# Optimization experiments

Measured on AMD Instinct MI355X. Metric: run time of the kernel, lower is better.

## Reference

```python
import jax, jax.numpy as jnp
import numpy as np

N_LEVELS = 127.0  # 2^(8-1)-1, symmetric signed int8


def _ste_round_clip(x, scale, lo, hi):
    """Fake-quantize x to integers in [lo,hi] at given scale, straight-through estimator."""
    q = jnp.clip(jnp.round(x / scale), lo, hi) * scale
    return x + jax.lax.stop_gradient(q - x)


def quant_act(x):
    """Per-tensor symmetric int8 activation quantization (QuantAct)."""
    scale = jax.lax.stop_gradient(jnp.max(jnp.abs(x)) / N_LEVELS)
    xq = _ste_round_clip(x, scale, -N_LEVELS - 1.0, N_LEVELS)
    return xq, scale


def quant_linear(xq, act_scale, w, b):
    """Per-tensor symmetric int8 weight quantization + bias quantized at act*weight scale (QuantLinear)."""
    w_scale = jax.lax.stop_gradient(jnp.max(jnp.abs(w)) / N_LEVELS)
    wq = _ste_round_clip(w, w_scale, -N_LEVELS, N_LEVELS)
    bias_scale = act_scale * w_scale
    bq = b + jax.lax.stop_gradient(jnp.round(b / bias_scale) * bias_scale - b)
    out = xq @ wq.T + bq  # equivalent to int8 GEMM accumulated in int32, dequantized
    return out, w_scale


def setup_inputs() -> dict:
    key = jax.random.key(0)
    ks = jax.random.split(key, 7)
    B, D_IN, D_H, D_OUT = 512, 9216, 4096, 1000  # AlexNet head dims
    s1 = 1.0 / np.sqrt(D_IN)
    s2 = 1.0 / np.sqrt(D_H)
    return {
        "x": jax.random.normal(ks[0], (B, D_IN), jnp.float32),
        "w1": jax.random.normal(ks[1], (D_H, D_IN), jnp.float32) * s1,
        "b1": jax.random.normal(ks[2], (D_H,), jnp.float32) * 0.01,
        "w2": jax.random.normal(ks[3], (D_H, D_H), jnp.float32) * s2,
        "b2": jax.random.normal(ks[4], (D_H,), jnp.float32) * 0.01,
        "w3": jax.random.normal(ks[5], (D_OUT, D_H), jnp.float32) * s2,
        "b3": jax.random.normal(ks[6], (D_OUT,), jnp.float32) * 0.01,
    }


def reference(x, w1, b1, w2, b2, w3, b3):
    # quant_act -> quant_fc1 -> ReLU -> (Dropout: eval=identity) -> quant_act1 -> quant_fc2 -> ReLU -> quant_act2 -> quant_fc3
    xq, a_s = quant_act(x)
    h, _ = quant_linear(xq, a_s, w1, b1)
    h = jax.nn.relu(h)
    hq, a_s = quant_act(h)
    h, _ = quant_linear(hq, a_s, w2, b2)
    h = jax.nn.relu(h)
    hq, a_s = quant_act(h)
    out, _ = quant_linear(hq, a_s, w3, b3)
    return out
```

## Files before the change

kernel.cpp:

```cpp
#include <hip/hip_runtime.h>
#include <hip/hip_bf16.h>

typedef __attribute__((ext_vector_type(4))) int   int32x4;
typedef __attribute__((ext_vector_type(4))) float float4v;


__global__ void init_stats(float* stats) {
    if (threadIdx.x < 64) stats[threadIdx.x] = 0.0f;
}

__global__ void maxabs_kernel(const float* __restrict__ src, long nchunk, float* __restrict__ out) {
    const int tid  = threadIdx.x;
    const int lane = tid & 63;
    const int wid  = tid >> 6;
    __shared__ float red[4];
    float m0 = 0.0f, m1 = 0.0f, m2 = 0.0f, m3 = 0.0f;
    for (long c = blockIdx.x; c < nchunk; c += gridDim.x) {
        const float4v* p = (const float4v*)src + c * 1024 + tid;
        float4v v0 = p[0], v1 = p[256], v2 = p[512], v3 = p[768];
        m0 = fmaxf(m0, fmaxf(fmaxf(fabsf(v0.x), fabsf(v0.y)), fmaxf(fabsf(v0.z), fabsf(v0.w))));
        m1 = fmaxf(m1, fmaxf(fmaxf(fabsf(v1.x), fabsf(v1.y)), fmaxf(fabsf(v1.z), fabsf(v1.w))));
        m2 = fmaxf(m2, fmaxf(fmaxf(fabsf(v2.x), fabsf(v2.y)), fmaxf(fabsf(v2.z), fabsf(v2.w))));
        m3 = fmaxf(m3, fmaxf(fmaxf(fabsf(v3.x), fabsf(v3.y)), fmaxf(fabsf(v3.z), fabsf(v3.w))));
    }
    float m = fmaxf(fmaxf(m0, m1), fmaxf(m2, m3));
    #pragma unroll
    for (int off = 32; off; off >>= 1) m = fmaxf(m, __shfl_xor(m, off, 64));
    if (lane == 0) red[wid] = m;
    __syncthreads();
    if (tid == 0) {
        float r = fmaxf(fmaxf(red[0], red[1]), fmaxf(red[2], red[3]));
        atomicMax((unsigned int*)out, __float_as_uint(r));
    }
}

__global__ void quant_kernel(const float* __restrict__ src, signed char* __restrict__ dst,
                             const float* __restrict__ stats, int slot,
                             float lo, float hi, long nchunk) {
    const float scale = stats[slot] / 127.0f;
    const int tid = threadIdx.x;
    for (long c = blockIdx.x; c < nchunk; c += gridDim.x) {
        const float4v* p = (const float4v*)src + c * 1024 + tid;
        int* d = (int*)dst + c * 1024 + tid;
        float4v v0 = p[0], v1 = p[256], v2 = p[512], v3 = p[768];
        float4v vs[4] = {v0, v1, v2, v3};
        int packed[4];
        #pragma unroll
        for (int j = 0; j < 4; ++j) {
            float4v v = vs[j];
            int b0 = (int)fminf(fmaxf(rintf(v.x / scale), lo), hi);
            int b1 = (int)fminf(fmaxf(rintf(v.y / scale), lo), hi);
            int b2 = (int)fminf(fmaxf(rintf(v.z / scale), lo), hi);
            int b3 = (int)fminf(fmaxf(rintf(v.w / scale), lo), hi);
            packed[j] = (b0 & 0xff) | ((b1 & 0xff) << 8) | ((b2 & 0xff) << 16) | ((b3 & 0xff) << 24);
        }
        d[0]   = packed[0];
        d[256] = packed[1];
        d[512] = packed[2];
        d[768] = packed[3];
    }
}

template <int BM, int BN, int FR, int FC, bool RELUMAX>
__global__ __launch_bounds__(256, 2)
void gemm_q8(const signed char* __restrict__ A, const signed char* __restrict__ Bw,
             const float* __restrict__ bias, float* __restrict__ stats,
             int a_slot, int w_slot, int h_slot,
             float* __restrict__ C, int K, int Ncols) {
    constexpr int BK = 64;
    constexpr int NWC = BN / (FC * 16);
    constexpr int L = BM / 64 + BN / 64;
    static_assert((BM / (FR * 16)) * (BN / (FC * 16)) == 4, "4 waves");
    constexpr int LDS_A = BM * BK;
    constexpr int LDS_TILE = (BM + BN) * BK;
    __shared__ __align__(16) signed char lds[3][LDS_TILE];

    const int tid  = threadIdx.x;
    const int wid  = tid >> 6;
    const int lane = tid & 63;
    const int wr   = wid / NWC;
    const int wc   = wid % NWC;

    const long brow = (long)blockIdx.y * BM;
    const long bcol = (long)blockIdx.x * BN;

    const signed char* Ab = A  + brow * K;
    const signed char* Bb = Bw + bcol * K;

    const int srow = tid >> 2;
    const int scb  = (tid & 3) * 16;
    const int scsrc = scb ^ (((srow >> 1) & 3) << 4);

    int32x4 zero = {0, 0, 0, 0};
    int32x4 acc[FR][FC];
    #pragma unroll
    for (int r = 0; r < FR; ++r)
        #pragma unroll
        for (int c = 0; c < FC; ++c) acc[r][c] = zero;

    auto stage = [&](int buf, int kt) {
        #pragma unroll
        for (int i = 0; i < BM / 64; ++i) {
            __builtin_amdgcn_global_load_lds(
                (const __attribute__((address_space(1))) void*)(Ab + (long)(srow + i * 64) * K + kt + scsrc),
                (__attribute__((address_space(3))) void*)(&lds[buf][(srow + i * 64) * BK + scb]),
                16, 0, 0);
        }
        #pragma unroll
        for (int i = 0; i < BN / 64; ++i) {
            __builtin_amdgcn_global_load_lds(
                (const __attribute__((address_space(1))) void*)(Bb + (long)(srow + i * 64) * K + kt + scsrc),
                (__attribute__((address_space(3))) void*)(&lds[buf][LDS_A + (srow + i * 64) * BK + scb]),
                16, 0, 0);
        }
    };

    const int nt = K / BK;
    stage(0, 0);
    if (nt > 1) stage(1, BK);

    for (int t = 0; t < nt; ++t) {
        if (t + 1 < nt) {
            asm volatile("s_waitcnt vmcnt(%0)\n\ts_barrier" :: "n"(L) : "memory");
        } else {
            asm volatile("s_waitcnt vmcnt(0)\n\ts_barrier" ::: "memory");
        }
        if (t + 2 < nt) stage((t + 2) % 3, (t + 2) * BK);

        const signed char* la = &lds[t % 3][0];
        const signed char* lb = &lds[t % 3][LDS_A];
        int32x4 af[FR], bf[FC];
        #pragma unroll
        for (int r = 0; r < FR; ++r) {
            const int row = wr * (FR * 16) + r * 16 + (lane & 15);
            const int col = ((lane >> 4) * 16) ^ (((row >> 1) & 3) << 4);
            af[r] = *(const int32x4*)(la + row * BK + col);
        }
        #pragma unroll
        for (int c = 0; c < FC; ++c) {
            const int row = wc * (FC * 16) + c * 16 + (lane & 15);
            const int col = ((lane >> 4) * 16) ^ (((row >> 1) & 3) << 4);
            bf[c] = *(const int32x4*)(lb + row * BK + col);
        }

        #pragma unroll
        for (int r = 0; r < FR; ++r)
            #pragma unroll
            for (int c = 0; c < FC; ++c)
                acc[r][c] = __builtin_amdgcn_mfma_i32_16x16x64_i8(af[r], bf[c], acc[r][c], 0, 0, 0);
    }

    const float sa = stats[a_slot] / 127.0f;
    const float sw = stats[w_slot] / 127.0f;
    const float s  = sa * sw;
    float lmax = 0.0f;
    #pragma unroll
    for (int c = 0; c < FC; ++c) {
        const long col = bcol + wc * (FC * 16) + c * 16 + (lane & 15);
        const bool colok = (col < Ncols);
        float bint = 0.0f;
        if (colok) bint = rintf(bias[col] / s);
        #pragma unroll
        for (int r = 0; r < FR; ++r) {
            #pragma unroll
            for (int j = 0; j < 4; ++j) {
                const long row = brow + wr * (FR * 16) + r * 16 + (lane >> 4) * 4 + j;
                float v = ((float)acc[r][c][j] + bint) * s;
                if (RELUMAX) v = fmaxf(v, 0.0f);
                if (colok) C[row * Ncols + col] = v;
                if (RELUMAX) lmax = fmaxf(lmax, v);
            }
        }
    }
    if (RELUMAX) {
        __shared__ float red[4];
        #pragma unroll
        for (int off = 32; off; off >>= 1) lmax = fmaxf(lmax, __shfl_xor(lmax, off, 64));
        if (lane == 0) red[wid] = lmax;
        __syncthreads();
        if (tid == 0) {
            float r = fmaxf(fmaxf(red[0], red[1]), fmaxf(red[2], red[3]));
            atomicMax((unsigned int*)&stats[h_slot], __float_as_uint(r));
        }
    }
}

static inline long lminl(long a, long b) { return a < b ? a : b; }

extern "C" void kernel_launch(void* const* d_in, const int* in_sizes, int n_in,
                              void* d_out, int out_size, void* d_ws, size_t ws_size,
                              hipStream_t stream) {
    const float* x  = (const float*)d_in[0];
    const float* w1 = (const float*)d_in[1];
    const float* b1 = (const float*)d_in[2];
    const float* w2 = (const float*)d_in[3];
    const float* b2 = (const float*)d_in[4];
    const float* w3 = (const float*)d_in[5];
    const float* b3 = (const float*)d_in[6];
    float* out = (float*)d_out;

    constexpr int B = 512, DIN = 9216, DH = 4096, DOUT = 1000;

    char* ws = (char*)d_ws;
    float*       stats = (float*)ws;
    signed char* xq    = (signed char*)(ws + 256);
    signed char* w1q   = xq  + (size_t)B * DIN;
    signed char* w2q   = w1q + (size_t)DH * DIN;
    signed char* w3q   = w2q + (size_t)DH * DH;
    signed char* h1q   = w3q + (size_t)1024 * DH;
    signed char* h2q   = h1q + (size_t)B * DH;
    float*       hbuf  = (float*)(h2q + (size_t)B * DH);
    const size_t need  = 256 + (size_t)B*DIN + (size_t)DH*DIN + (size_t)DH*DH + (size_t)1024*DH
                       + 2*(size_t)B*DH + (size_t)B*DH*4;
    if (ws_size < need) return;

    init_stats<<<1, 64, 0, stream>>>(stats);

    auto launch_maxabs = [&](const float* p, long n, int slot) {
        long nchunk = n / 4096;
        int blocks = (int)lminl(nchunk, 2048);
        maxabs_kernel<<<blocks, 256, 0, stream>>>(p, nchunk, stats + slot);
    };
    auto launch_quant = [&](const float* p, signed char* q, long n, int slot, float lo) {
        long nchunk = n / 4096;
        int blocks = (int)lminl(nchunk, 2048);
        quant_kernel<<<blocks, 256, 0, stream>>>(p, q, stats, slot, lo, 127.0f, nchunk);
    };

    launch_maxabs(x, (long)B * DIN, 0);
    launch_quant(x, xq, (long)B * DIN, 0, -128.0f);
    launch_maxabs(w1, (long)DH * DIN, 1);
    launch_quant(w1, w1q, (long)DH * DIN, 1, -127.0f);
    launch_maxabs(w2, (long)DH * DH, 2);
    launch_quant(w2, w2q, (long)DH * DH, 2, -127.0f);
    launch_maxabs(w3, (long)DOUT * DH, 3);
    launch_quant(w3, w3q, (long)DOUT * DH, 3, -127.0f);

    gemm_q8<64, 128, 2, 4, true><<<dim3(DH / 128, B / 64), 256, 0, stream>>>(
        xq, w1q, b1, stats, 0, 1, 4, hbuf, DIN, DH);
    launch_quant(hbuf, h1q, (long)B * DH, 4, -128.0f);

    gemm_q8<64, 128, 2, 4, true><<<dim3(DH / 128, B / 64), 256, 0, stream>>>(
        h1q, w2q, b2, stats, 4, 2, 5, hbuf, DH, DH);
    launch_quant(hbuf, h2q, (long)B * DH, 5, -128.0f);

    gemm_q8<64, 64, 2, 2, false><<<dim3(16, B / 64), 256, 0, stream>>>(
        h2q, w3q, b3, stats, 5, 3, 0, out, DH, DOUT);
}
```

Baseline: 545.0 us.

## Split-K int8 GEMMs with atomic int32 accumulation and separate epilogue kernels

Each GEMM now splits K four ways across gridDim.z and accumulates int32 partials into a zeroed workspace with atomicAdd. Separate finish kernels then apply the bias, dequantize, run ReLU and compute the max-abs statistic. The goal is more blocks to fill the GPU, since the grids were only 256 and 128 blocks before, and launch_bounds are raised for occupancy. The cost is extra zeroing and finish passes, heavy atomic traffic on the output, and more launches.

```diff
diff --git a/kernel.cpp b/kernel.cpp
--- a/kernel.cpp
+++ b/kernel.cpp
@@ -7,6 +7,13 @@
 
 __global__ void init_stats(float* stats) {
     if (threadIdx.x < 64) stats[threadIdx.x] = 0.0f;
+}
+
+__global__ void zero_kernel(int32x4* __restrict__ p, long n4) {
+    long i = (long)blockIdx.x * blockDim.x + threadIdx.x;
+    long stride = (long)gridDim.x * blockDim.x;
+    int32x4 z = {0, 0, 0, 0};
+    for (; i < n4; i += stride) p[i] = z;
 }
 
 __global__ void maxabs_kernel(const float* __restrict__ src, long nchunk, float* __restrict__ out) {
@@ -61,12 +68,10 @@
     }
 }
 
-template <int BM, int BN, int FR, int FC, bool RELUMAX>
-__global__ __launch_bounds__(256, 2)
+template <int BM, int BN, int FR, int FC>
+__global__ __launch_bounds__(256, 4)
 void gemm_q8(const signed char* __restrict__ A, const signed char* __restrict__ Bw,
-             const float* __restrict__ bias, float* __restrict__ stats,
-             int a_slot, int w_slot, int h_slot,
-             float* __restrict__ C, int K, int Ncols) {
+             int* __restrict__ Acc, int K, int kslice, int ldacc) {
     constexpr int BK = 64;
     constexpr int NWC = BN / (FC * 16);
     constexpr int L = BM / 64 + BN / 64;
@@ -81,11 +86,12 @@
     const int wr   = wid / NWC;
     const int wc   = wid % NWC;
 
-    const long brow = (long)blockIdx.y * BM;
-    const long bcol = (long)blockIdx.x * BN;
-
-    const signed char* Ab = A  + brow * K;
-    const signed char* Bb = Bw + bcol * K;
+    const int brow  = blockIdx.y * BM;
+    const int bcol  = blockIdx.x * BN;
+    const int kbase = blockIdx.z * kslice;
+
+    const signed char* Ab = A  + (long)brow * K + kbase;
+    const signed char* Bb = Bw + (long)bcol * K + kbase;
 
     const int srow = tid >> 2;
     const int scb  = (tid & 3) * 16;
@@ -115,7 +121,7 @@
         }
     };
 
-    const int nt = K / BK;
+    const int nt = kslice / BK;
     stage(0, 0);
     if (nt > 1) stage(1, BK);
 
@@ -150,38 +156,62 @@
                 acc[r][c] = __builtin_amdgcn_mfma_i32_16x16x64_i8(af[r], bf[c], acc[r][c], 0, 0, 0);
     }
 
-    const float sa = stats[a_slot] / 127.0f;
-    const float sw = stats[w_slot] / 127.0f;
-    const float s  = sa * sw;
+    #pragma unroll
+    for (int c = 0; c < FC; ++c) {
+        const int col = bcol + wc * (FC * 16) + c * 16 + (lane & 15);
+        #pragma unroll
+        for (int r = 0; r < FR; ++r) {
+            const int row0 = brow + wr * (FR * 16) + r * 16 + (lane >> 4) * 4;
+            #pragma unroll
+            for (int j = 0; j < 4; ++j)
+                atomicAdd(&Acc[(long)(row0 + j) * ldacc + col], acc[r][c][j]);
+        }
+    }
+}
+
+__global__ void finish_relu_kernel(int* __restrict__ buf, const float* __restrict__ bias,
+                                   float* __restrict__ stats, int a_slot, int w_slot, int h_slot,
+                                   long n4, int colmask) {
+    const float s = (stats[a_slot] / 127.0f) * (stats[w_slot] / 127.0f);
+    const int tid = threadIdx.x;
+    const int lane = tid & 63;
+    const int wid = tid >> 6;
+    __shared__ float red[4];
     float lmax = 0.0f;
-    #pragma unroll
-    for (int c = 0; c < FC; ++c) {
-        const long col = bcol + wc * (FC * 16) + c * 16 + (lane & 15);
-        const bool colok = (col < Ncols);
-        float bint = 0.0f;
-        if (colok) bint = rintf(bias[col] / s);
-        #pragma unroll
-        for (int r = 0; r < FR; ++r) {
-            #pragma unroll
-            for (int j = 0; j < 4; ++j) {
-                const long row = brow + wr * (FR * 16) + r * 16 + (lane >> 4) * 4 + j;
-                float v = ((float)acc[r][c][j] + bint) * s;
-                if (RELUMAX) v = fmaxf(v, 0.0f);
-                if (colok) C[row * Ncols + col] = v;
-                if (RELUMAX) lmax = fmaxf(lmax, v);
-            }
-        }
-    }
-    if (RELUMAX) {
-        __shared__ float red[4];
-        #pragma unroll
-        for (int off = 32; off; off >>= 1) lmax = fmaxf(lmax, __shfl_xor(lmax, off, 64));
-        if (lane == 0) red[wid] = lmax;
-        __syncthreads();
-        if (tid == 0) {
-            float r = fmaxf(fmaxf(red[0], red[1]), fmaxf(red[2], red[3]));
-            atomicMax((unsigned int*)&stats[h_slot], __float_as_uint(r));
-        }
+    long i = (long)blockIdx.x * blockDim.x + tid;
+    long stride = (long)gridDim.x * blockDim.x;
+    for (; i < n4; i += stride) {
+        int32x4 a = ((int32x4*)buf)[i];
+        float4v v;
+        #pragma unroll
+        for (int j = 0; j < 4; ++j) {
+            int col = (int)((i * 4 + j) & colmask);
+            float bint = rintf(bias[col] / s);
+            float val = ((float)a[j] + bint) * s;
+            val = fmaxf(val, 0.0f);
+            v[j] = val;
+            lmax = fmaxf(lmax, val);
+        }
+        ((float4v*)buf)[i] = v;
+    }
+    #pragma unroll
+    for (int off = 32; off; off >>= 1) lmax = fmaxf(lmax, __shfl_xor(lmax, off, 64));
+    if (lane == 0) red[wid] = lmax;
+    __syncthreads();
+    if (tid == 0) {
+        float r = fmaxf(fmaxf(red[0], red[1]), fmaxf(red[2], red[3]));
+        atomicMax((unsigned int*)&stats[h_slot], __float_as_uint(r));
+    }
+}
+
+__global__ void finish3_kernel(const int* __restrict__ acc, const float* __restrict__ bias,
+                               const float* __restrict__ stats, int a_slot, int w_slot,
+                               float* __restrict__ out, int ncols) {
+    const float s = (stats[a_slot] / 127.0f) * (stats[w_slot] / 127.0f);
+    const int row = blockIdx.x;
+    for (int col = threadIdx.x; col < ncols; col += blockDim.x) {
+        float bint = rintf(bias[col] / s);
+        out[(long)row * ncols + col] = ((float)acc[(long)row * 1024 + col] + bint) * s;
     }
 }
 
@@ -236,14 +266,23 @@
     launch_maxabs(w3, (long)DOUT * DH, 3);
     launch_quant(w3, w3q, (long)DOUT * DH, 3, -127.0f);
 
-    gemm_q8<64, 128, 2, 4, true><<<dim3(DH / 128, B / 64), 256, 0, stream>>>(
-        xq, w1q, b1, stats, 0, 1, 4, hbuf, DIN, DH);
+    int* acc = (int*)hbuf;
+    const long n4_h = (long)B * DH / 4;
+
+    zero_kernel<<<2048, 256, 0, stream>>>((int32x4*)acc, n4_h);
+    gemm_q8<64, 128, 2, 4><<<dim3(DH / 128, B / 64, 4), 256, 0, stream>>>(
+        xq, w1q, acc, DIN, DIN / 4, DH);
+    finish_relu_kernel<<<2048, 256, 0, stream>>>(acc, b1, stats, 0, 1, 4, n4_h, DH - 1);
     launch_quant(hbuf, h1q, (long)B * DH, 4, -128.0f);
 
-    gemm_q8<64, 128, 2, 4, true><<<dim3(DH / 128, B / 64), 256, 0, stream>>>(
-        h1q, w2q, b2, stats, 4, 2, 5, hbuf, DH, DH);
+    zero_kernel<<<2048, 256, 0, stream>>>((int32x4*)acc, n4_h);
+    gemm_q8<64, 128, 2, 4><<<dim3(DH / 128, B / 64, 4), 256, 0, stream>>>(
+        h1q, w2q, acc, DH, DH / 4, DH);
+    finish_relu_kernel<<<2048, 256, 0, stream>>>(acc, b2, stats, 4, 2, 5, n4_h, DH - 1);
     launch_quant(hbuf, h2q, (long)B * DH, 5, -128.0f);
 
-    gemm_q8<64, 64, 2, 2, false><<<dim3(16, B / 64), 256, 0, stream>>>(
-        h2q, w3q, b3, stats, 5, 3, 0, out, DH, DOUT);
-}
+    zero_kernel<<<512, 256, 0, stream>>>((int32x4*)acc, (long)B * 1024 / 4);
+    gemm_q8<64, 64, 2, 2><<<dim3(16, B / 64, 4), 256, 0, stream>>>(
+        h2q, w3q, acc, DH, DH / 4, 1024);
+    finish3_kernel<<<B, 256, 0, stream>>>(acc, b3, stats, 5, 3, out, DOUT);
+}
```

Result: no change. 549.2 us (+0.8%).
